# Optimization experiments

Measured on AMD Instinct MI355X. Metric: run time of the kernel, lower is better.

## Reference

```python
import jax, jax.numpy as jnp
import numpy as np

N_NODES = 100_000
N_CH = 16
DIM = 3
N_EDGES = 1_600_000
N_STEPS = 2
MAX_STEP_LEN = 1.0
EPS = jnp.float32(jnp.finfo(jnp.float32).eps)  # orig uses float64 eps; fp32-safe here


def setup_inputs() -> dict:
    key = jax.random.key(0)
    k1, k2, k3, k4, k5 = jax.random.split(key, 5)
    nodes = jax.random.normal(k1, (N_NODES, N_CH, DIM), dtype=jnp.float32)
    nodes = nodes / jnp.linalg.norm(nodes, axis=-1, keepdims=True)  # project to S^2
    senders = jax.random.randint(k2, (N_EDGES,), 0, N_NODES, dtype=jnp.int32)
    receivers = jax.random.randint(k3, (N_EDGES,), 0, N_NODES, dtype=jnp.int32)
    weights = jnp.ones((N_EDGES,), dtype=jnp.float32)
    # mimic truncated_normal(std=1)+1 inits (squared later => positive params)
    t_sqrt = 1.0 + 0.5 * jax.random.normal(k4, (N_CH,), dtype=jnp.float32)
    alpha_sqrt = 1.0 + 0.5 * jax.random.normal(k5, (N_CH,), dtype=jnp.float32)
    beta_sqrt = jnp.ones((N_CH,), dtype=jnp.float32)
    return dict(nodes=nodes, senders=senders, receivers=receivers, weights=weights,
                t_sqrt=t_sqrt, alpha_sqrt=alpha_sqrt, beta_sqrt=beta_sqrt)


def sphere_log(x, y):
    # log_x(y) on the unit sphere; x, y: (..., DIM)
    c = jnp.clip(jnp.sum(x * y, axis=-1, keepdims=True), -1.0 + 1e-7, 1.0 - 1e-7)
    theta = jnp.arccos(c)
    return (theta / jnp.sin(theta)) * (y - c * x)


def sphere_exp(x, v):
    # exp_x(v) on the unit sphere
    n = jnp.sqrt(jnp.sum(v * v, axis=-1, keepdims=True) + 1e-16)
    return jnp.cos(n) * x + (jnp.sin(n) / n) * v


def mfdg_laplace(nodes, senders, receivers, weights):
    # degree-normalized manifold graph Laplacian:
    #   L(x)_i = -(1/deg_i) * sum_{j in N(i)} w_ij log_{x_i}(x_j)
    logs = sphere_log(nodes[senders], nodes[receivers])         # (E, C, D)
    agg = jax.ops.segment_sum(weights[:, None, None] * logs, senders,
                              num_segments=N_NODES)             # (N, C, D)
    deg = jax.ops.segment_sum(weights, senders, num_segments=N_NODES)
    return -agg / (deg[:, None, None] + 1e-12)


def _flow(nodes, senders, receivers, weights, t_sqrt, alpha_sqrt, beta_sqrt):
    t = (t_sqrt ** 2) / N_STEPS   # (C,)
    a = alpha_sqrt ** 2           # (C,)
    b = beta_sqrt ** 2            # (C,)
    x = nodes
    for _ in range(N_STEPS):
        v = mfdg_laplace(x, senders, receivers, weights)        # (N, C, D)
        nrm = jnp.sqrt(jnp.sum(v * v, axis=-1) + EPS)           # (N, C)
        d = jax.nn.sigmoid(b * (nrm - a))                       # sigmoid gating
        scale = jnp.where(nrm * d <= MAX_STEP_LEN, d, MAX_STEP_LEN / nrm)
        v = -(v * scale[..., None]) * t[None, :, None]
        x = sphere_exp(x, v)
    return x


def reference(nodes, senders, receivers, weights, t_sqrt, alpha_sqrt, beta_sqrt):
    return _flow(nodes, senders, receivers, weights, t_sqrt, alpha_sqrt, beta_sqrt)
```

## Files before the change

kernel.cpp:

```cpp
#include <hip/hip_runtime.h>

#define N_NODES 100000
#define N_CH 16
#define DIM 3
#define N_EDGES 1600000
#define N_STEPS 2
#define EPS_D 1.1920928955078125e-7

#define PB 1024
#define NBLK ((N_NODES + PB - 1) / PB)
#define DBINS 64
#define NBUCK 256
#define TA 4096
#define NBLK_A ((N_EDGES + TA - 1) / TA)
#define NBLK_B 2048

__global__ void hist_kernel(const int4* __restrict__ senders4,
                            int* __restrict__ cnt) {
    int e = blockIdx.x * blockDim.x + threadIdx.x;
    if (e < N_EDGES / 4) {
        int4 s = senders4[e];
        atomicAdd(&cnt[s.x], 1);
        atomicAdd(&cnt[s.y], 1);
        atomicAdd(&cnt[s.z], 1);
        atomicAdd(&cnt[s.w], 1);
    }
}

__global__ void scan_partials_dhist(const int* __restrict__ cnt,
                                    int* __restrict__ part,
                                    int* __restrict__ bins) {
    __shared__ int sh[PB];
    __shared__ int lb[DBINS];
    int t = threadIdx.x;
    if (t < DBINS) lb[t] = 0;
    int g = blockIdx.x * PB + t;
    int v = (g < N_NODES) ? cnt[g] : 0;
    sh[t] = v;
    __syncthreads();
    for (int off = PB / 2; off > 0; off >>= 1) {
        if (t < off) sh[t] += sh[t + off];
        __syncthreads();
    }
    if (t == 0) part[blockIdx.x] = sh[0];
    if (g < N_NODES) {
        int d = (v > DBINS - 1) ? (DBINS - 1) : v;
        atomicAdd(&lb[d], 1);
    }
    __syncthreads();
    if (t < DBINS && lb[t]) atomicAdd(&bins[t], lb[t]);
}

__global__ void scan_mid_fused(int* __restrict__ part,
                               int* __restrict__ rowptr,
                               const int* __restrict__ bins,
                               int* __restrict__ binoff,
                               int* __restrict__ binfill) {
    __shared__ int sh[128];
    int t = threadIdx.x;
    int v = (t < NBLK) ? part[t] : 0;
    sh[t] = v;
    __syncthreads();
    for (int off = 1; off < 128; off <<= 1) {
        int u = (t >= off) ? sh[t - off] : 0;
        __syncthreads();
        sh[t] += u;
        __syncthreads();
    }
    if (t < NBLK) part[t] = sh[t] - v;
    if (t == NBLK - 1) rowptr[N_NODES] = sh[t];
    if (t < DBINS) {
        int bv = bins[t];
        int s = bv;
        for (int off = 1; off < DBINS; off <<= 1) {
            int u = __shfl_up(s, off, 64);
            if (t >= off) s += u;
        }
        binoff[t] = s - bv;
        binfill[t] = 0;
    }
}

__global__ void scan_apply_dscatter(const int* __restrict__ cnt,
                                    const int* __restrict__ part,
                                    int* __restrict__ rowptr,
                                    const int* __restrict__ binoff,
                                    int* __restrict__ binfill,
                                    int* __restrict__ perm,
                                    int* __restrict__ bfill) {
    __shared__ int sh[PB];
    __shared__ int lcnt[DBINS];
    __shared__ int lbase[DBINS];
    int t = threadIdx.x;
    if (t < DBINS) lcnt[t] = 0;
    int g = blockIdx.x * PB + t;
    int v = (g < N_NODES) ? cnt[g] : 0;
    sh[t] = v;
    __syncthreads();
    for (int off = 1; off < PB; off <<= 1) {
        int u = (t >= off) ? sh[t - off] : 0;
        __syncthreads();
        sh[t] += u;
        __syncthreads();
    }
    if (g < N_NODES) {
        int rp = part[blockIdx.x] + sh[t] - v;
        rowptr[g] = rp;
        if ((g & 511) == 0) bfill[g >> 9] = rp;
    }
    int d = 0, myoff = 0;
    if (g < N_NODES) {
        d = (v > DBINS - 1) ? (DBINS - 1) : v;
        myoff = atomicAdd(&lcnt[d], 1);
    }
    __syncthreads();
    if (t < DBINS && lcnt[t]) lbase[t] = atomicAdd(&binfill[t], lcnt[t]);
    __syncthreads();
    if (g < N_NODES && perm) perm[binoff[d] + lbase[d] + myoff] = g;
}

__global__ void bucket_scatter(const int* __restrict__ senders,
                               const int* __restrict__ receivers,
                               const float* __restrict__ weights,
                               int* __restrict__ bfill,
                               int* __restrict__ stg_s,
                               int2* __restrict__ stg_rw) {
    __shared__ int lcnt[NBUCK];
    __shared__ int lbase[NBUCK];
    int t = threadIdx.x;
    lcnt[t] = 0;
    __syncthreads();
    int base = blockIdx.x * TA;
    for (int k = t; k < TA; k += 256) {
        int e = base + k;
        if (e < N_EDGES) atomicAdd(&lcnt[senders[e] >> 9], 1);
    }
    __syncthreads();
    int c = lcnt[t];
    if (c) lbase[t] = atomicAdd(&bfill[t], c);
    __syncthreads();
    lcnt[t] = 0;
    __syncthreads();
    for (int k = t; k < TA; k += 256) {
        int e = base + k;
        if (e < N_EDGES) {
            int s = senders[e];
            int b = s >> 9;
            int pos = lbase[b] + atomicAdd(&lcnt[b], 1);
            stg_s[pos] = s;
            stg_rw[pos] = make_int2(receivers[e], __float_as_int(weights[e]));
        }
    }
}

__global__ void fine_scatter(const int* __restrict__ stg_s,
                             const int2* __restrict__ stg_rw,
                             const int* __restrict__ rowptr,
                             int* __restrict__ cnt,
                             int2* __restrict__ edata) {
    const int CH = (N_EDGES + NBLK_B - 1) / NBLK_B;
    int bid = blockIdx.x;
    int chunk = (bid & 7) * (NBLK_B / 8) + (bid >> 3);
    int s0 = chunk * CH;
    int s1 = s0 + CH; if (s1 > N_EDGES) s1 = N_EDGES;
    for (int e = s0 + (int)threadIdx.x; e < s1; e += 256) {
        int s = stg_s[e];
        int old = atomicAdd(&cnt[s], -1);
        edata[rowptr[s] + old - 1] = stg_rw[e];
    }
}

__device__ __forceinline__ double fast_rsqrt(double x) {
    double y = (double)rsqrtf((float)x);
    y = y * fma(-0.5 * x, y * y, 1.5);
    return y;
}

__device__ __forceinline__ double theta_over_sin(double cd) {
    double acd = fabs(cd);
    bool mid = (acd <= 0.5);
    double z = mid ? (cd * cd) : (0.5 * (1.0 - acd));
    double A = 0.008390335809943149;
    A = fma(A, z, 0.009761609529194078);
    A = fma(A, z, 0.011551800896139706);
    A = fma(A, z, 0.013964843750);
    A = fma(A, z, 0.017352764423076924);
    A = fma(A, z, 0.022372159090909092);
    A = fma(A, z, 0.030381944444444444);
    A = fma(A, z, 0.044642857142857144);
    A = fma(A, z, 0.075);
    A = fma(A, z, 0.16666666666666666);
    A = fma(A, z, 1.0);
    double R = fast_rsqrt(1.0 - z);
    if (mid) return (1.5707963267948966 - cd * A) * R;
    double AR = A * R;
    if (cd > 0.0) return AR;
    double Rz = fast_rsqrt(z);
    return fma(1.5707963267948966 * Rz, R, -AR);
}

template <typename TI, typename TO>
__global__ void flow_kernel(const TI* __restrict__ x,
                            const int* __restrict__ rowptr,
                            const int2* __restrict__ edata,
                            const int* __restrict__ perm,
                            const float* __restrict__ t_sqrt,
                            const float* __restrict__ alpha_sqrt,
                            const float* __restrict__ beta_sqrt,
                            TO* __restrict__ xout) {
    int wave = threadIdx.x >> 6;
    int lane = threadIdx.x & 63;
    int q = lane >> 4;
    int c = lane & 15;
    int slot = (blockIdx.x * 4 + wave) * 4 + q;
    int i = perm ? perm[slot] : slot;

    int beg = rowptr[i];
    int end = rowptr[i + 1];

    const TI* xi = x + ((size_t)i * N_CH + c) * DIM;
    double ax = (double)xi[0], ay = (double)xi[1], az = (double)xi[2];

    double sx = 0.0, sy = 0.0, sz = 0.0, sw = 0.0;
    for (int k = beg; k < end; ++k) {
        int2 ed = edata[k];
        int r = ed.x;
        double w = (double)__int_as_float(ed.y);
        const TI* xr = x + ((size_t)r * N_CH + c) * DIM;
        double bx = (double)xr[0], by = (double)xr[1], bz = (double)xr[2];

        double cd = ax * bx + ay * by + az * bz;
        cd = fmin(fmax(cd, -1.0 + 1e-7), 1.0 - 1e-7);
        double f = w * theta_over_sin(cd);

        sx += f * (bx - cd * ax);
        sy += f * (by - cd * ay);
        sz += f * (bz - cd * az);
        sw += w;
    }

    double dg = sw + 1e-12;
    double inv = 1.0 / dg;
    double vx = -sx * inv, vy = -sy * inv, vz = -sz * inv;

    double t = (double)t_sqrt[c];     t = (t * t) / (double)N_STEPS;
    double a = (double)alpha_sqrt[c]; a = a * a;
    double b = (double)beta_sqrt[c];  b = b * b;

    double nrm = sqrt(vx * vx + vy * vy + vz * vz + EPS_D);
    double d = 1.0 / (1.0 + exp(-b * (nrm - a)));
    double scale = (nrm * d <= 1.0) ? d : (1.0 / nrm);
    double fs = -scale * t;
    vx *= fs; vy *= fs; vz *= fs;

    double n = sqrt(vx * vx + vy * vy + vz * vz + 1e-16);
    double cn = cos(n);
    double sf = sin(n) / n;

    TO* xo = xout + ((size_t)i * N_CH + c) * DIM;
    xo[0] = (TO)(cn * ax + sf * vx);
    xo[1] = (TO)(cn * ay + sf * vy);
    xo[2] = (TO)(cn * az + sf * vz);
}

__global__ void deg_kernel(const int* __restrict__ senders,
                           const float* __restrict__ weights,
                           float* __restrict__ deg) {
    int e = blockIdx.x * blockDim.x + threadIdx.x;
    if (e < N_EDGES) atomicAdd(&deg[senders[e]], weights[e]);
}

__global__ void edge_kernel(const float* __restrict__ x,
                            const int* __restrict__ senders,
                            const int* __restrict__ receivers,
                            const float* __restrict__ weights,
                            float* __restrict__ agg) {
    unsigned int tid = blockIdx.x * blockDim.x + threadIdx.x;
    if (tid >= (unsigned int)N_EDGES * N_CH) return;
    unsigned int e = tid >> 4;
    unsigned int c = tid & 15u;
    int s = senders[e];
    int r = receivers[e];
    float w = weights[e];
    const float* xs = x + ((size_t)s * N_CH + c) * DIM;
    const float* xr = x + ((size_t)r * N_CH + c) * DIM;
    float ax = xs[0], ay = xs[1], az = xs[2];
    float bx = xr[0], by = xr[1], bz = xr[2];
    float cd = ax * bx + ay * by + az * bz;
    cd = fminf(fmaxf(cd, -1.0f + 1e-7f), 1.0f - 1e-7f);
    float theta = acosf(cd);
    float sn = sqrtf(fmaxf(1.0f - cd * cd, 0.0f));
    float f = w * theta / sn;
    float* ag = agg + ((size_t)s * N_CH + c) * DIM;
    atomicAdd(&ag[0], f * (bx - cd * ax));
    atomicAdd(&ag[1], f * (by - cd * ay));
    atomicAdd(&ag[2], f * (bz - cd * az));
}

__global__ void node_kernel(const float* __restrict__ xin,
                            const float* __restrict__ agg,
                            const float* __restrict__ deg,
                            const float* __restrict__ t_sqrt,
                            const float* __restrict__ alpha_sqrt,
                            const float* __restrict__ beta_sqrt,
                            float* __restrict__ xout) {
    unsigned int tid = blockIdx.x * blockDim.x + threadIdx.x;
    if (tid >= (unsigned int)N_NODES * N_CH) return;
    unsigned int i = tid >> 4;
    unsigned int c = tid & 15u;
    float dg = deg[i] + 1e-12f;
    const float* ag = agg + (size_t)tid * DIM;
    float vx = -ag[0] / dg, vy = -ag[1] / dg, vz = -ag[2] / dg;
    float t = t_sqrt[c]; t = (t * t) * (1.0f / N_STEPS);
    float a = alpha_sqrt[c]; a = a * a;
    float b = beta_sqrt[c]; b = b * b;
    float nrm = sqrtf(vx * vx + vy * vy + vz * vz + 1.1920929e-7f);
    float d = 1.0f / (1.0f + __expf(-b * (nrm - a)));
    float scale = (nrm * d <= 1.0f) ? d : (1.0f / nrm);
    float fs = -scale * t;
    vx *= fs; vy *= fs; vz *= fs;
    const float* xi = xin + (size_t)tid * DIM;
    float axx = xi[0], ayy = xi[1], azz = xi[2];
    float n = sqrtf(vx * vx + vy * vy + vz * vz + 1e-16f);
    float cn = cosf(n);
    float sf = sinf(n) / n;
    float* xo = xout + (size_t)tid * DIM;
    xo[0] = cn * axx + sf * vx;
    xo[1] = cn * ayy + sf * vy;
    xo[2] = cn * azz + sf * vz;
}

extern "C" void kernel_launch(void* const* d_in, const int* in_sizes, int n_in,
                              void* d_out, int out_size, void* d_ws, size_t ws_size,
                              hipStream_t stream) {
    const float* nodes      = (const float*)d_in[0];
    const int*   senders    = (const int*)d_in[1];
    const int*   receivers  = (const int*)d_in[2];
    const float* weights    = (const float*)d_in[3];
    const float* t_sqrt     = (const float*)d_in[4];
    const float* alpha_sqrt = (const float*)d_in[5];
    const float* beta_sqrt  = (const float*)d_in[6];
    float* out = (float*)d_out;

    const size_t AL = 255;
    const size_t xtmp_b   = (size_t)N_NODES * N_CH * DIM * sizeof(double);
    const size_t rowptr_b = (((size_t)(N_NODES + 1) * sizeof(int)) + AL) & ~AL;
    const size_t cnt_b    = (((size_t)N_NODES * sizeof(int)) + AL) & ~AL;
    const size_t bins_b   = 2048;
    const size_t part_b   = 4096;
    const size_t perm_b   = (((size_t)N_NODES * sizeof(int)) + AL) & ~AL;
    const size_t edata_b  = (size_t)N_EDGES * sizeof(int2);
    const size_t need_sorted = xtmp_b + rowptr_b + cnt_b + bins_b + part_b + perm_b + edata_b;
    const size_t need_plain  = xtmp_b + rowptr_b + cnt_b + bins_b + part_b + edata_b;

    if (ws_size >= need_plain) {
        bool sorted = (ws_size >= need_sorted);
        char* p = (char*)d_ws;
        double* xtmp  = (double*)p;           p += xtmp_b;
        int*   rowptr = (int*)p;              p += rowptr_b;
        int*   cnt    = (int*)p;              p += cnt_b;
        int*   bins   = (int*)p;
        int*   binoff = bins + 64;
        int*   binfill= bins + 128;
        int*   bfill  = bins + 192;           p += bins_b;
        int*   part   = (int*)p;              p += part_b;
        int*   perm   = nullptr;
        if (sorted) { perm = (int*)p;         p += perm_b; }
        int2*  edata  = (int2*)p;

        int2*  stg_rw = (int2*)xtmp;
        int*   stg_s  = (int*)((char*)xtmp + edata_b);

        hipMemsetAsync(cnt, 0, cnt_b + 256, stream);
        hist_kernel<<<(N_EDGES / 4 + 255) / 256, 256, 0, stream>>>(
            (const int4*)senders, cnt);
        scan_partials_dhist<<<NBLK, PB, 0, stream>>>(cnt, part, bins);
        scan_mid_fused<<<1, 128, 0, stream>>>(part, rowptr, bins, binoff, binfill);
        scan_apply_dscatter<<<NBLK, PB, 0, stream>>>(cnt, part, rowptr,
                                                     binoff, binfill, perm, bfill);
        bucket_scatter<<<NBLK_A, NBUCK, 0, stream>>>(senders, receivers, weights,
                                                     bfill, stg_s, stg_rw);
        fine_scatter<<<NBLK_B, 256, 0, stream>>>(stg_s, stg_rw, rowptr, cnt, edata);

        int grid = N_NODES / 16;
        flow_kernel<float, double><<<grid, 256, 0, stream>>>(
            nodes, rowptr, edata, perm, t_sqrt, alpha_sqrt, beta_sqrt, xtmp);
        flow_kernel<double, float><<<grid, 256, 0, stream>>>(
            xtmp, rowptr, edata, perm, t_sqrt, alpha_sqrt, beta_sqrt, out);
    } else {
        float* agg = (float*)d_ws;
        float* deg = agg + (size_t)N_NODES * N_CH * DIM;
        hipMemsetAsync(deg, 0, N_NODES * sizeof(float), stream);
        deg_kernel<<<(N_EDGES + 255) / 256, 256, 0, stream>>>(senders, weights, deg);
        const float* xin = nodes;
        for (int step = 0; step < N_STEPS; ++step) {
            hipMemsetAsync(agg, 0, (size_t)N_NODES * N_CH * DIM * sizeof(float), stream);
            unsigned int n_ec = (unsigned int)N_EDGES * N_CH;
            edge_kernel<<<(n_ec + 255) / 256, 256, 0, stream>>>(xin, senders, receivers,
                                                                weights, agg);
            unsigned int n_nc = (unsigned int)N_NODES * N_CH;
            node_kernel<<<(n_nc + 255) / 256, 256, 0, stream>>>(xin, agg, deg, t_sqrt,
                                                                alpha_sqrt, beta_sqrt, out);
            xin = out;
        }
    }
}
```

Before: 354.7 us.

## Replace global-atomic fine scatter with per-bucket shared-memory counting sort

The second pass of the CSR build now uses one block per 512-node bucket instead of scattering every edge into the output with a global atomic decrement. Each block ranks its edges with shared-memory atomics, stages them in a shared buffer and writes the bucket's segment of edata contiguously. This removes global atomics and random global writes. In exchange only about 196 blocks run at one block per CU, with roughly 112KB of LDS each, and buckets larger than the capacity fall back to the old global-atomic path.

```diff
diff --git a/kernel.cpp b/kernel.cpp
--- a/kernel.cpp
+++ b/kernel.cpp
@@ -11,9 +11,10 @@
 #define NBLK ((N_NODES + PB - 1) / PB)
 #define DBINS 64
 #define NBUCK 256
+#define NBUCK_LIVE ((N_NODES + 511) / 512)
 #define TA 4096
 #define NBLK_A ((N_EDGES + TA - 1) / TA)
-#define NBLK_B 2048
+#define CAP 14336
 
 __global__ void hist_kernel(const int4* __restrict__ senders4,
                             int* __restrict__ cnt) {
@@ -153,20 +154,40 @@
     }
 }
 
-__global__ void fine_scatter(const int* __restrict__ stg_s,
-                             const int2* __restrict__ stg_rw,
-                             const int* __restrict__ rowptr,
-                             int* __restrict__ cnt,
-                             int2* __restrict__ edata) {
-    const int CH = (N_EDGES + NBLK_B - 1) / NBLK_B;
-    int bid = blockIdx.x;
-    int chunk = (bid & 7) * (NBLK_B / 8) + (bid >> 3);
-    int s0 = chunk * CH;
-    int s1 = s0 + CH; if (s1 > N_EDGES) s1 = N_EDGES;
-    for (int e = s0 + (int)threadIdx.x; e < s1; e += 256) {
-        int s = stg_s[e];
-        int old = atomicAdd(&cnt[s], -1);
-        edata[rowptr[s] + old - 1] = stg_rw[e];
+__global__ void __launch_bounds__(256, 1)
+bucket_sort(const int* __restrict__ stg_s,
+            const int2* __restrict__ stg_rw,
+            const int* __restrict__ rowptr,
+            int* __restrict__ cnt,
+            int2* __restrict__ edata) {
+    __shared__ int lcnt[512];
+    __shared__ int2 lrw[CAP];
+    int b = blockIdx.x;
+    int nbase = b << 9;
+    int nend = nbase + 512; if (nend > N_NODES) nend = N_NODES;
+    int ebase = rowptr[nbase];
+    int eend = rowptr[nend];
+    int m = eend - ebase;
+    int t = threadIdx.x;
+
+    if (m <= CAP) {
+        for (int k = t; k < 512; k += 256) lcnt[k] = 0;
+        __syncthreads();
+        for (int k = t; k < m; k += 256) {
+            int s = stg_s[ebase + k];
+            int rank = atomicAdd(&lcnt[s - nbase], 1);
+            lrw[(rowptr[s] - ebase) + rank] = stg_rw[ebase + k];
+        }
+        __syncthreads();
+        for (int k = t; k < m; k += 256) {
+            edata[ebase + k] = lrw[k];
+        }
+    } else {
+        for (int k = t; k < m; k += 256) {
+            int s = stg_s[ebase + k];
+            int old = atomicAdd(&cnt[s], -1);
+            edata[rowptr[s] + old - 1] = stg_rw[ebase + k];
+        }
     }
 }
 
@@ -380,7 +401,7 @@
                                                      binoff, binfill, perm, bfill);
         bucket_scatter<<<NBLK_A, NBUCK, 0, stream>>>(senders, receivers, weights,
                                                      bfill, stg_s, stg_rw);
-        fine_scatter<<<NBLK_B, 256, 0, stream>>>(stg_s, stg_rw, rowptr, cnt, edata);
+        bucket_sort<<<NBUCK_LIVE, 256, 0, stream>>>(stg_s, stg_rw, rowptr, cnt, edata);
 
         int grid = N_NODES / 16;
         flow_kernel<float, double><<<grid, 256, 0, stream>>>(
```

Result: faster. 333.5 us (-6.0%).
